# Kernel tuning notes

Hardware: AMD Instinct MI355X
Metric: run time of the kernel (lower is better)

The kernel has to match this reference:

```python
import jax, jax.numpy as jnp
import numpy as np

NE, NR = 200000, 500
D, TRI_H, TET_H = 128, 256, 256
NTRI, NTET = 500000, 200000
B = 8192
E_ET, E_TT, E_ETT = 1500000, 800000, 800000


def _mean_aggregate(src_idx, dst_idx, src, num_dst):
    # scatter-add of gathered messages, then divide by per-dst counts (0 -> 0)
    agg = jax.ops.segment_sum(src[src_idx], dst_idx, num_segments=num_dst)
    cnt = jax.ops.segment_sum(jnp.ones(src_idx.shape[0], dtype=src.dtype), dst_idx, num_segments=num_dst)
    return jnp.where((cnt > 0)[:, None], agg / jnp.maximum(cnt, 1.0)[:, None], 0.0)


def _layernorm(x, w, b, eps=1e-5):
    mu = jnp.mean(x, axis=-1, keepdims=True)
    var = jnp.mean((x - mu) ** 2, axis=-1, keepdims=True)
    return (x - mu) / jnp.sqrt(var + eps) * w + b


def setup_inputs():
    key = jax.random.key(0)
    ks = jax.random.split(key, 24)
    def xav(k, fan_out, fan_in):
        a = np.sqrt(6.0 / (fan_in + fan_out))
        return jax.random.uniform(k, (fan_out, fan_in), jnp.float32, -a, a)
    inp = {
        'entity_emb': xav(ks[0], NE, D),
        'relation_emb': xav(ks[1], NR, D),
        'g2_w1': xav(ks[2], TRI_H, D), 'g2_b1': jnp.zeros((TRI_H,), jnp.float32),
        'g2_w2': xav(ks[3], TRI_H, TRI_H), 'g2_b2': jnp.zeros((TRI_H,), jnp.float32),
        'g3_w1': xav(ks[4], TET_H, TRI_H), 'g3_b1': jnp.zeros((TET_H,), jnp.float32),
        'g3_w2': xav(ks[5], TET_H, TET_H), 'g3_b2': jnp.zeros((TET_H,), jnp.float32),
        'te_w': xav(ks[6], D, TET_H), 'te_b': jnp.zeros((D,), jnp.float32),
        'ln_w': jnp.ones((D,), jnp.float32), 'ln_b': jnp.zeros((D,), jnp.float32),
        'fusion_alpha': jnp.zeros((2,), jnp.float32),
        'gamma': jnp.array([12.0], jnp.float32),
        'triples': jax.random.randint(ks[7], (B, 3), 0, NR, jnp.int64 if jax.config.jax_enable_x64 else jnp.int32),
        'et_index': jax.random.randint(ks[8], (2, E_ET), 0, NE, jnp.int32),
        'tt_index': jax.random.randint(ks[9], (2, E_TT), 0, NTET, jnp.int32),
        'ent_tet_index': jax.random.randint(ks[10], (2, E_ETT), 0, NTET, jnp.int32),
        'num_triangles': NTRI,
        'num_tetras': NTET,
    }
    return inp


def reference(entity_emb, relation_emb, g2_w1, g2_b1, g2_w2, g2_b2,
              g3_w1, g3_b1, g3_w2, g3_b2, te_w, te_b, ln_w, ln_b,
              fusion_alpha, gamma, triples, et_index, tt_index,
              ent_tet_index, num_triangles, num_tetras):
    # gnn2: entity -> triangle  (segment-mean then Linear -> GELU -> Linear)
    tri_agg = _mean_aggregate(et_index[0], et_index[1], entity_emb, num_triangles)
    tri = jax.nn.gelu(tri_agg @ g2_w1.T + g2_b1, approximate=False) @ g2_w2.T + g2_b2
    # gnn3: triangle -> tetra
    tet_agg = _mean_aggregate(tt_index[0], tt_index[1], tri, num_tetras)
    tet = jax.nn.gelu(tet_agg @ g3_w1.T + g3_b1, approximate=False) @ g3_w2.T + g3_b2
    # project tetra -> entity dim, then tetra -> entity mean-aggregate (swapped index rows)
    tet_proj = tet @ te_w.T + te_b
    v_topo = _mean_aggregate(ent_tet_index[1], ent_tet_index[0], tet_proj, entity_emb.shape[0])
    v_topo = _layernorm(v_topo, ln_w, ln_b)
    # learned fusion
    w = jax.nn.softmax(fusion_alpha)
    V = w[0] * entity_emb + w[1] * v_topo
    # TransE scoring: gamma - ||V[h] + R[r] - V[t]||_2
    h, r, t = triples[:, 0], triples[:, 1], triples[:, 2]
    diff = V[h] + relation_emb[r] - V[t]
    return gamma[0] - jnp.sqrt(jnp.sum(diff * diff, axis=-1))
```

## Files before the change

### kernel.cpp

```cpp
#include <hip/hip_runtime.h>
#include <cmath>

#define NE_     200000
#define NR_     500
#define D_      128
#define TRIH_   256
#define TETH_   256
#define NTRI_   500000
#define NTET_   200000
#define B_      8192
#define EET_    1500000
#define ETT_    800000
#define EETT_   800000

#define CAP_V   2048
#define CAP_TP  8192
#define CAP_TRI 12288

#define LCAP_ET  131072
#define LCAP_TT  32768
#define LCAP_ETT 16384

#define COARSEN 8
#define CHUNK   (256 * COARSEN)

#define NBC_V   ((NE_   + CHUNK - 1) / CHUNK)
#define NBC_TP  ((NTET_ + CHUNK - 1) / CHUNK)
#define NBC_TRI ((NTRI_ + CHUNK - 1) / CHUNK)
#define NBF_ET  ((EET_  + CHUNK - 1) / CHUNK)
#define NBF_TT  ((ETT_  + CHUNK - 1) / CHUNK)
#define NBF_ETT ((EETT_ + CHUNK - 1) / CHUNK)
#define MARKB   1024


typedef float f32x4 __attribute__((ext_vector_type(4)));
typedef short s16x8 __attribute__((ext_vector_type(8)));

__device__ __forceinline__ float gelu_exact(float v) {
    return 0.5f * v * (1.0f + erff(v * 0.70710678118654752f));
}

__device__ __forceinline__ unsigned short f2bf(float f) {
    unsigned int u = __float_as_uint(f);
    unsigned int r = (u + 0x7fffu + ((u >> 16) & 1u)) >> 16;
    return (unsigned short)r;
}

__device__ __forceinline__ int wave_rank_emit(bool pred, int* lcnt, int lane) {
    unsigned long long mask = __ballot(pred);
    int rank = __popcll(mask & ((1ull << lane) - 1ull));
    int total = __popcll(mask);
    int wb = 0;
    if (lane == 0 && total) wb = atomicAdd(lcnt, total);
    wb = __shfl(wb, 0, 64);
    return pred ? (wb + rank) : -1;
}


__global__ void k_init_all(int* __restrict__ id_v, int* __restrict__ id_tp,
                           int* __restrict__ id_tri, int* __restrict__ ctr,
                           const float* __restrict__ w1, const float* __restrict__ w2,
                           const float* __restrict__ w3, const float* __restrict__ w4,
                           const float* __restrict__ w5, unsigned short* __restrict__ wb,
                           int* __restrict__ deg_tri, int* __restrict__ deg_tp,
                           int* __restrict__ deg_v) {
    int i = blockIdx.x * blockDim.x + threadIdx.x;
    int st = gridDim.x * blockDim.x;
    for (int x = i; x < NE_; x += st) id_v[x] = -1;
    for (int x = i; x < NTET_; x += st) id_tp[x] = -1;
    for (int x = i; x < NTRI_; x += st) id_tri[x] = -1;
    if (i < 16) ctr[i] = 0;
    for (int x = i; x < 262144; x += st) {
        float f;
        if (x < 32768)       f = w1[x];
        else if (x < 98304)  f = w2[x - 32768];
        else if (x < 163840) f = w3[x - 98304];
        else if (x < 229376) f = w4[x - 163840];
        else                 f = w5[x - 229376];
        wb[x] = f2bf(f);
    }
    for (int x = i; x < CAP_TRI; x += st) deg_tri[x] = 0;
    for (int x = i; x < CAP_TP; x += st) deg_tp[x] = 0;
    for (int x = i; x < CAP_V; x += st) deg_v[x] = 0;
}


__global__ void k_mark_v(const int* __restrict__ triples, int* __restrict__ id_v) {
    int b = blockIdx.x * blockDim.x + threadIdx.x;
    if (b >= B_) return;
    id_v[triples[b * 3 + 0]] = -2;
    id_v[triples[b * 3 + 2]] = -2;
}

__global__ void k_mark_tp(const int* __restrict__ ett, const int* __restrict__ id_v,
                          int* __restrict__ id_tp) {
    int i = blockIdx.x * blockDim.x + threadIdx.x;
    int st = gridDim.x * blockDim.x;
    for (int e = i; e < EETT_; e += st)
        if (id_v[ett[e]] != -1) id_tp[ett[EETT_ + e]] = -2;
}


__device__ void do_compact(int* __restrict__ arr, int n, int* __restrict__ g, int cap,
                           int bid, int* lcnt, int* lbase) {
    if (threadIdx.x == 0) *lcnt = 0;
    __syncthreads();
    const int lane = threadIdx.x & 63;
    const int base = bid * CHUNK;
    int pos[COARSEN];
#pragma unroll
    for (int u = 0; u < COARSEN; ++u) {
        int e = base + u * 256 + threadIdx.x;
        bool pred = (e < n) && (arr[e] == -2);
        pos[u] = wave_rank_emit(pred, lcnt, lane);
    }
    __syncthreads();
    if (threadIdx.x == 0) *lbase = *lcnt ? atomicAdd(g, *lcnt) : 0;
    __syncthreads();
    const int b0 = *lbase;
#pragma unroll
    for (int u = 0; u < COARSEN; ++u) {
        if (pos[u] >= 0) {
            int e = base + u * 256 + threadIdx.x;
            int idx = b0 + pos[u];
            arr[e] = (idx < cap) ? idx : -1;
        }
    }
}

__device__ void do_filter(const int* __restrict__ e0, const int* __restrict__ e1,
                          const int* __restrict__ map0, const int* __restrict__ map1,
                          int n, int2* __restrict__ list, int* __restrict__ nctr, int lcap,
                          int* __restrict__ deg, int bid, int* lcnt, int* lbase) {
    if (threadIdx.x == 0) *lcnt = 0;
    __syncthreads();
    const int lane = threadIdx.x & 63;
    const int base = bid * CHUNK;
    int pos[COARSEN]; int2 val[COARSEN];
#pragma unroll
    for (int u = 0; u < COARSEN; ++u) {
        int e = base + u * 256 + threadIdx.x;
        bool pred = false;
        int m1 = -1, src = -1;
        if (e < n) {
            m1 = map1[e1[e]];
            if (m1 >= 0) {
                src = map0 ? map0[e0[e]] : e0[e];
                pred = (src >= 0);
            }
        }
        pos[u] = wave_rank_emit(pred, lcnt, lane);
        if (pred) { val[u] = make_int2(src, m1); atomicAdd(&deg[m1], 1); }
    }
    __syncthreads();
    if (threadIdx.x == 0) *lbase = *lcnt ? atomicAdd(nctr, *lcnt) : 0;
    __syncthreads();
    const int b0 = *lbase;
#pragma unroll
    for (int u = 0; u < COARSEN; ++u)
        if (pos[u] >= 0 && b0 + pos[u] < lcap) list[b0 + pos[u]] = val[u];
}

__launch_bounds__(256)
__global__ void k_p4(const int* __restrict__ tt, int* __restrict__ id_v,
                     int* __restrict__ id_tp, int* __restrict__ id_tri,
                     int* __restrict__ ctr) {
    __shared__ int lcnt, lbase;
    int bid = blockIdx.x;
    if (bid < NBC_V) { do_compact(id_v, NE_, &ctr[0], CAP_V, bid, &lcnt, &lbase); return; }
    bid -= NBC_V;
    if (bid < NBC_TP) { do_compact(id_tp, NTET_, &ctr[1], CAP_TP, bid, &lcnt, &lbase); return; }
    bid -= NBC_TP;
    int i = bid * 256 + threadIdx.x;
    int st = MARKB * 256;
    for (int e = i; e < ETT_; e += st)
        if (id_tp[tt[ETT_ + e]] != -1) id_tri[tt[e]] = -2;
}

__launch_bounds__(256)
__global__ void k_p5(int* __restrict__ id_tri, const int* __restrict__ ett,
                     const int* __restrict__ id_v, const int* __restrict__ id_tp,
                     int2* __restrict__ list_ett, int* __restrict__ deg_v,
                     int* __restrict__ ctr) {
    __shared__ int lcnt, lbase;
    int bid = blockIdx.x;
    if (bid < NBC_TRI) { do_compact(id_tri, NTRI_, &ctr[2], CAP_TRI, bid, &lcnt, &lbase); return; }
    bid -= NBC_TRI;
    do_filter(ett + EETT_, ett, id_tp, id_v, EETT_, list_ett, &ctr[5], LCAP_ETT,
              deg_v, bid, &lcnt, &lbase);
}

__launch_bounds__(256)
__global__ void k_p6(const int* __restrict__ et, const int* __restrict__ tt,
                     const int* __restrict__ id_tri, const int* __restrict__ id_tp,
                     int2* __restrict__ list_et, int2* __restrict__ list_tt,
                     int* __restrict__ deg_tri, int* __restrict__ deg_tp,
                     int* __restrict__ ctr) {
    __shared__ int lcnt, lbase;
    int bid = blockIdx.x;
    if (bid < NBF_ET) {
        do_filter(et, et + EET_, nullptr, id_tri, EET_, list_et, &ctr[3], LCAP_ET,
                  deg_tri, bid, &lcnt, &lbase);
        return;
    }
    bid -= NBF_ET;
    do_filter(tt, tt + ETT_, id_tri, id_tp, ETT_, list_tt, &ctr[4], LCAP_TT,
              deg_tp, bid, &lcnt, &lbase);
}


__device__ void scan_level(const int* __restrict__ deg, int* __restrict__ start,
                           int* __restrict__ cur, int n) {
    __shared__ int wsum[16];
    const int tid = threadIdx.x;
    const int per = (n + 1023) >> 10;
    const int base = tid * per;
    int s = 0;
    for (int k = 0; k < per; ++k) { int i = base + k; if (i < n) s += deg[i]; }
    const int lane = tid & 63, wid = tid >> 6;
    int v = s;
#pragma unroll
    for (int o = 1; o < 64; o <<= 1) { int t = __shfl_up(v, o, 64); if (lane >= o) v += t; }
    if (lane == 63) wsum[wid] = v;
    __syncthreads();
    if (tid < 16) {
        int w = wsum[tid];
#pragma unroll
        for (int o = 1; o < 16; o <<= 1) { int t = __shfl_up(w, o, 64); if (tid >= o) w += t; }
        wsum[tid] = w;
    }
    __syncthreads();
    int run = v - s + (wid > 0 ? wsum[wid - 1] : 0);
    for (int k = 0; k < per; ++k) {
        int i = base + k;
        if (i < n) { start[i] = run; cur[i] = run; run += deg[i]; }
    }
    if (tid == 0) start[n] = wsum[15];
}

__global__ void k_scan(const int* __restrict__ deg_tri, int* __restrict__ st_tri, int* __restrict__ cu_tri,
                       const int* __restrict__ deg_tp, int* __restrict__ st_tp, int* __restrict__ cu_tp,
                       const int* __restrict__ deg_v, int* __restrict__ st_v, int* __restrict__ cu_v) {
    if (blockIdx.x == 0)      scan_level(deg_tri, st_tri, cu_tri, CAP_TRI);
    else if (blockIdx.x == 1) scan_level(deg_tp, st_tp, cu_tp, CAP_TP);
    else                      scan_level(deg_v, st_v, cu_v, CAP_V);
}

__global__ void k_bucket(const int* __restrict__ ctr,
                         const int2* __restrict__ le, int* __restrict__ cu_tri, int* __restrict__ be,
                         const int2* __restrict__ lt, int* __restrict__ cu_tp, int* __restrict__ btk,
                         const int2* __restrict__ lv, int* __restrict__ cu_v, int* __restrict__ bv) {
    int i = blockIdx.x * blockDim.x + threadIdx.x;
    int st = gridDim.x * blockDim.x;
    int n0 = min(ctr[3], LCAP_ET);
    for (int e = i; e < n0; e += st) {
        int2 p = le[e];
        int slot = atomicAdd(&cu_tri[p.y], 1);
        if (slot < LCAP_ET) be[slot] = p.x;
    }
    int n1 = min(ctr[4], LCAP_TT);
    for (int e = i; e < n1; e += st) {
        int2 p = lt[e];
        int slot = atomicAdd(&cu_tp[p.y], 1);
        if (slot < LCAP_TT) btk[slot] = p.x;
    }
    int n2 = min(ctr[5], LCAP_ETT);
    for (int e = i; e < n2; e += st) {
        int2 p = lv[e];
        int slot = atomicAdd(&cu_v[p.y], 1);
        if (slot < LCAP_ETT) bv[slot] = p.x;
    }
}


template<int W>
__global__ void k_gather(const int* __restrict__ ctrp, int cidx, int cap, int lcap,
                         const int* __restrict__ start, const int* __restrict__ bidx,
                         const float* __restrict__ src, unsigned srcN,
                         float* __restrict__ dst, float* __restrict__ cnt) {
    const int c = min(ctrp[cidx], cap);
    const int lane = threadIdx.x & 63;
    int row = (blockIdx.x * blockDim.x + threadIdx.x) >> 6;
    const int nw = (gridDim.x * blockDim.x) >> 6;
    for (; row < c; row += nw) {
        int s0 = min(start[row], lcap), s1 = min(start[row + 1], lcap);
        if (W == 128) {
            float2 acc = make_float2(0.f, 0.f);
            for (int e = s0; e < s1; ++e) {
                unsigned si = (unsigned)bidx[e];
                if (si < srcN) {
                    float2 v = ((const float2*)(src + (size_t)si * 128))[lane];
                    acc.x += v.x; acc.y += v.y;
                }
            }
            ((float2*)(dst + (size_t)row * 128))[lane] = acc;
        } else {
            float4 acc = make_float4(0.f, 0.f, 0.f, 0.f);
            for (int e = s0; e < s1; ++e) {
                unsigned si = (unsigned)bidx[e];
                if (si < srcN) {
                    float4 v = ((const float4*)(src + (size_t)si * 256))[lane];
                    acc.x += v.x; acc.y += v.y; acc.z += v.z; acc.w += v.w;
                }
            }
            ((float4*)(dst + (size_t)row * 256))[lane] = acc;
        }
        if (lane == 0) cnt[row] = (float)(s1 - s0);
    }
}


template<int K, int ACT, bool DIV>
__launch_bounds__(256)
__global__ void k_gemm(const int* __restrict__ ctrp, int ctr_idx, int cap,
                       const float* __restrict__ A, const float* __restrict__ cnt,
                       const unsigned short* __restrict__ Wb, const float* __restrict__ bias,
                       float* __restrict__ C, int N) {
    constexpr int KU = K / 8;
    __shared__ uint4 lA[32 * KU];
    __shared__ uint4 lW[32 * KU];
    __shared__ float invs[32];
    const int c = min(ctrp[ctr_idx], cap);
    const int row0 = blockIdx.x * 32;
    if (row0 >= c) return;
    const int tid = threadIdx.x;
    const int gc0 = blockIdx.y * 32;

    if (DIV) {
        if (tid < 32) {
            int gr = row0 + tid;
            float cc = (gr < c) ? cnt[gr] : 0.0f;
            invs[tid] = (cc > 0.0f) ? 1.0f / cc : 0.0f;
        }
        __syncthreads();
    }
#pragma unroll
    for (int it = 0; it < KU / 8; ++it) {
        int u = tid + it * 256;
        int r = u / KU, ku = u % KU;
        const float* src = &A[(size_t)(row0 + r) * K + ku * 8];
        float4 f0 = *(const float4*)src;
        float4 f1 = *(const float4*)(src + 4);
        float m = DIV ? invs[r] : 1.0f;
        s16x8 v;
        v[0] = (short)f2bf(f0.x * m); v[1] = (short)f2bf(f0.y * m);
        v[2] = (short)f2bf(f0.z * m); v[3] = (short)f2bf(f0.w * m);
        v[4] = (short)f2bf(f1.x * m); v[5] = (short)f2bf(f1.y * m);
        v[6] = (short)f2bf(f1.z * m); v[7] = (short)f2bf(f1.w * m);
        *(s16x8*)&lA[r * KU + (ku ^ (r & 7))] = v;
    }
#pragma unroll
    for (int it = 0; it < KU / 8; ++it) {
        int u = tid + it * 256;
        int r = u / KU, ku = u % KU;
        lW[r * KU + (ku ^ (r & 7))] = *(const uint4*)&Wb[(size_t)(gc0 + r) * K + ku * 8];
    }
    __syncthreads();

    const int w = tid >> 6, l = tid & 63;
    const int wr = (w >> 1) * 16, wc = (w & 1) * 16;
    const int fr = l & 15, fo = l >> 4;
    f32x4 acc = {0.0f, 0.0f, 0.0f, 0.0f};
    const uint4* pa = &lA[(wr + fr) * KU];
    const uint4* pb = &lW[(wc + fr) * KU];
    const int sa = fr & 7, sb = fr & 7;
#pragma unroll
    for (int kk = 0; kk < K / 32; ++kk) {
        s16x8 a = *(const s16x8*)&pa[(kk * 4 + fo) ^ sa];
        s16x8 b = *(const s16x8*)&pb[(kk * 4 + fo) ^ sb];
        acc = __builtin_amdgcn_mfma_f32_16x16x32_bf16(a, b, acc, 0, 0, 0);
    }
    const int gcol = gc0 + wc + fr;
    const float bb = bias[gcol];
#pragma unroll
    for (int j = 0; j < 4; ++j) {
        int grow = row0 + wr + fo * 4 + j;
        if (grow < c) {
            float v = acc[j] + bb;
            if (ACT == 1) v = gelu_exact(v);
            C[(size_t)grow * N + gcol] = v;
        }
    }
}


__global__ void k_final(const float* __restrict__ emb, const float* __restrict__ rel,
                        const float* __restrict__ v_topo, const float* __restrict__ cnt_v,
                        const int* __restrict__ id_v, const float* __restrict__ ln_w,
                        const float* __restrict__ ln_b, const float* __restrict__ alpha,
                        const float* __restrict__ gamma, const int* __restrict__ triples,
                        float* __restrict__ out) {
    const int lane = threadIdx.x & 63;
    const int b = blockIdx.x * 4 + (threadIdx.x >> 6);
    if (b >= B_) return;
    float a0 = alpha[0], a1 = alpha[1];
    float m = fmaxf(a0, a1);
    float e0 = expf(a0 - m), e1 = expf(a1 - m);
    float w0 = e0 / (e0 + e1), w1 = e1 / (e0 + e1);
    int h = triples[b * 3 + 0];
    int r = triples[b * 3 + 1];
    int t = triples[b * 3 + 2];
    int jh = max(id_v[h], 0);
    int jt = max(id_v[t], 0);
    const float2* vt2 = (const float2*)v_topo;
    float2 rh = vt2[(size_t)jh * 64 + lane];
    float2 rt = vt2[(size_t)jt * 64 + lane];
    float chn = cnt_v[jh], ctn = cnt_v[jt];
    float ih = (chn > 0.f) ? 1.f / chn : 0.f;
    float it_ = (ctn > 0.f) ? 1.f / ctn : 0.f;
    float2 xh = make_float2(rh.x * ih, rh.y * ih);
    float2 xt = make_float2(rt.x * it_, rt.y * it_);
    float sh = xh.x + xh.y, st = xt.x + xt.y;
#pragma unroll
    for (int o = 32; o >= 1; o >>= 1) { sh += __shfl_xor(sh, o, 64); st += __shfl_xor(st, o, 64); }
    float muh = sh * (1.f / 128.f), mut = st * (1.f / 128.f);
    float2 dh = make_float2(xh.x - muh, xh.y - muh);
    float2 dt = make_float2(xt.x - mut, xt.y - mut);
    float vh_ = dh.x * dh.x + dh.y * dh.y, vt_ = dt.x * dt.x + dt.y * dt.y;
#pragma unroll
    for (int o = 32; o >= 1; o >>= 1) { vh_ += __shfl_xor(vh_, o, 64); vt_ += __shfl_xor(vt_, o, 64); }
    float rsh = rsqrtf(vh_ * (1.f / 128.f) + 1e-5f);
    float rst = rsqrtf(vt_ * (1.f / 128.f) + 1e-5f);
    float2 lw = ((const float2*)ln_w)[lane];
    float2 lb = ((const float2*)ln_b)[lane];
    float2 lnh = make_float2(dh.x * rsh * lw.x + lb.x, dh.y * rsh * lw.y + lb.y);
    float2 lnt = make_float2(dt.x * rst * lw.x + lb.x, dt.y * rst * lw.y + lb.y);
    float2 eh = ((const float2*)emb)[(size_t)h * 64 + lane];
    float2 etv = ((const float2*)emb)[(size_t)t * 64 + lane];
    float2 rr = ((const float2*)rel)[(size_t)r * 64 + lane];
    float dx = (w0 * eh.x + w1 * lnh.x) + rr.x - (w0 * etv.x + w1 * lnt.x);
    float dy = (w0 * eh.y + w1 * lnh.y) + rr.y - (w0 * etv.y + w1 * lnt.y);
    float ss = dx * dx + dy * dy;
#pragma unroll
    for (int o = 32; o >= 1; o >>= 1) ss += __shfl_xor(ss, o, 64);
    if (lane == 0) out[b] = gamma[0] - sqrtf(ss);
}


extern "C" void kernel_launch(void* const* d_in, const int* in_sizes, int n_in,
                              void* d_out, int out_size, void* d_ws, size_t ws_size,
                              hipStream_t stream) {
    const float* entity_emb = (const float*)d_in[0];
    const float* relation_emb = (const float*)d_in[1];
    const float* g2_w1 = (const float*)d_in[2];
    const float* g2_b1 = (const float*)d_in[3];
    const float* g2_w2 = (const float*)d_in[4];
    const float* g2_b2 = (const float*)d_in[5];
    const float* g3_w1 = (const float*)d_in[6];
    const float* g3_b1 = (const float*)d_in[7];
    const float* g3_w2 = (const float*)d_in[8];
    const float* g3_b2 = (const float*)d_in[9];
    const float* te_w = (const float*)d_in[10];
    const float* te_b = (const float*)d_in[11];
    const float* ln_w = (const float*)d_in[12];
    const float* ln_b = (const float*)d_in[13];
    const float* alpha = (const float*)d_in[14];
    const float* gamma = (const float*)d_in[15];
    const int* triples = (const int*)d_in[16];
    const int* et = (const int*)d_in[17];
    const int* tt = (const int*)d_in[18];
    const int* ett = (const int*)d_in[19];
    float* out = (float*)d_out;

    char* base = (char*)d_ws;
    size_t off = 0;
    auto take = [&](size_t bytes) -> void* {
        void* p = base + off;
        off = (off + bytes + 255) & ~(size_t)255;
        return p;
    };
    int* id_v = (int*)take((size_t)NE_ * 4);
    int* id_tp = (int*)take((size_t)NTET_ * 4);
    int* id_tri = (int*)take((size_t)NTRI_ * 4);
    int* ctr = (int*)take(64);
    int* deg_tri = (int*)take((size_t)CAP_TRI * 4);
    int* deg_tp = (int*)take((size_t)CAP_TP * 4);
    int* deg_v = (int*)take((size_t)CAP_V * 4);
    int* st_tri = (int*)take((size_t)(CAP_TRI + 1) * 4);
    int* st_tp = (int*)take((size_t)(CAP_TP + 1) * 4);
    int* st_v = (int*)take((size_t)(CAP_V + 1) * 4);
    int* cu_tri = (int*)take((size_t)CAP_TRI * 4);
    int* cu_tp = (int*)take((size_t)CAP_TP * 4);
    int* cu_v = (int*)take((size_t)CAP_V * 4);
    float* cnt_tri = (float*)take((size_t)CAP_TRI * 4);
    float* cnt_tp = (float*)take((size_t)CAP_TP * 4);
    float* cnt_v = (float*)take((size_t)CAP_V * 4);
    float* tri_agg = (float*)take((size_t)CAP_TRI * D_ * 4);
    float* h_tri = (float*)take((size_t)CAP_TRI * TRIH_ * 4);
    float* tri_c = (float*)take((size_t)CAP_TRI * TRIH_ * 4);
    float* tet_agg = (float*)take((size_t)CAP_TP * TRIH_ * 4);
    float* h_tet = (float*)take((size_t)CAP_TP * TETH_ * 4);
    float* tet_proj = (float*)take((size_t)CAP_TP * D_ * 4);
    float* v_topo = (float*)take((size_t)CAP_V * D_ * 4);
    unsigned short* wb = (unsigned short*)take((size_t)262144 * 2);
    int2* list_et = (int2*)take((size_t)LCAP_ET * 8);
    int2* list_tt = (int2*)take((size_t)LCAP_TT * 8);
    int2* list_ett = (int2*)take((size_t)LCAP_ETT * 8);
    int* b_et = (int*)take((size_t)LCAP_ET * 4);
    int* b_tt = (int*)take((size_t)LCAP_TT * 4);
    int* b_ett = (int*)take((size_t)LCAP_ETT * 4);
    if (off > ws_size) return;

    float* y_tet = h_tri;
    const unsigned short* wb_g2w1 = wb;
    const unsigned short* wb_g2w2 = wb + 32768;
    const unsigned short* wb_g3w1 = wb + 98304;
    const unsigned short* wb_g3w2 = wb + 163840;
    const unsigned short* wb_te   = wb + 229376;

    k_init_all<<<2048, 256, 0, stream>>>(id_v, id_tp, id_tri, ctr,
                                         g2_w1, g2_w2, g3_w1, g3_w2, te_w, wb,
                                         deg_tri, deg_tp, deg_v);
    k_mark_v<<<(B_ + 255) / 256, 256, 0, stream>>>(triples, id_v);
    k_mark_tp<<<MARKB, 256, 0, stream>>>(ett, id_v, id_tp);
    k_p4<<<NBC_V + NBC_TP + MARKB, 256, 0, stream>>>(tt, id_v, id_tp, id_tri, ctr);
    k_p5<<<NBC_TRI + NBF_ETT, 256, 0, stream>>>(id_tri, ett, id_v, id_tp, list_ett, deg_v, ctr);
    k_p6<<<NBF_ET + NBF_TT, 256, 0, stream>>>(et, tt, id_tri, id_tp, list_et, list_tt,
                                              deg_tri, deg_tp, ctr);
    k_scan<<<3, 1024, 0, stream>>>(deg_tri, st_tri, cu_tri, deg_tp, st_tp, cu_tp,
                                   deg_v, st_v, cu_v);
    k_bucket<<<256, 256, 0, stream>>>(ctr, list_et, cu_tri, b_et,
                                      list_tt, cu_tp, b_tt, list_ett, cu_v, b_ett);

    k_gather<128><<<2048, 256, 0, stream>>>(ctr, 2, CAP_TRI, LCAP_ET, st_tri, b_et,
                                            entity_emb, NE_, tri_agg, cnt_tri);
    dim3 gtri(CAP_TRI / 32, TRIH_ / 32);
    k_gemm<128, 1, true><<<gtri, 256, 0, stream>>>(ctr, 2, CAP_TRI, tri_agg, cnt_tri,
                                                   wb_g2w1, g2_b1, h_tri, TRIH_);
    k_gemm<256, 0, false><<<gtri, 256, 0, stream>>>(ctr, 2, CAP_TRI, h_tri, nullptr,
                                                    wb_g2w2, g2_b2, tri_c, TRIH_);
    k_gather<256><<<512, 256, 0, stream>>>(ctr, 1, CAP_TP, LCAP_TT, st_tp, b_tt,
                                           tri_c, CAP_TRI, tet_agg, cnt_tp);
    dim3 gtet(CAP_TP / 32, TETH_ / 32);
    k_gemm<256, 1, true><<<gtet, 256, 0, stream>>>(ctr, 1, CAP_TP, tet_agg, cnt_tp,
                                                   wb_g3w1, g3_b1, h_tet, TETH_);
    k_gemm<256, 0, false><<<gtet, 256, 0, stream>>>(ctr, 1, CAP_TP, h_tet, nullptr,
                                                    wb_g3w2, g3_b2, y_tet, TETH_);
    dim3 gproj(CAP_TP / 32, D_ / 32);
    k_gemm<256, 0, false><<<gproj, 256, 0, stream>>>(ctr, 1, CAP_TP, y_tet, nullptr,
                                                     wb_te, te_b, tet_proj, D_);
    k_gather<128><<<128, 256, 0, stream>>>(ctr, 0, CAP_V, LCAP_ETT, st_v, b_ett,
                                           tet_proj, CAP_TP, v_topo, cnt_v);
    k_final<<<(B_ + 3) / 4, 256, 0, stream>>>(entity_emb, relation_emb, v_topo, cnt_v, id_v,
                                              ln_w, ln_b, alpha, gamma, triples, out);
}
```

Measured before the change: 135.8 us.

## Assign compact ids via CAS and fuse MLP stages into fewer kernels

The mark-then-compact passes over full entity, tetra and triangle arrays are replaced by atomicCAS-based on-the-fly id assignment, which removes the chunked compaction kernels. The three edge filters are merged into one launch. The triangle MLP (two GEMMs with GELU) is fused into one kernel that keeps the hidden tile in LDS. The tetra gather plus its two GEMMs and the projection are fused into one kernel, and the final entity gather moves into the scoring kernel. Fused kernels recompute the first-layer hidden tile for every output column block, and the CAS assignment makes id order nondeterministic and adds atomic contention.

```diff
diff --git a/kernel.cpp b/kernel.cpp
--- a/kernel.cpp
+++ b/kernel.cpp
@@ -23,14 +23,16 @@
 
 #define COARSEN 8
 #define CHUNK   (256 * COARSEN)
-
-#define NBC_V   ((NE_   + CHUNK - 1) / CHUNK)
-#define NBC_TP  ((NTET_ + CHUNK - 1) / CHUNK)
-#define NBC_TRI ((NTRI_ + CHUNK - 1) / CHUNK)
 #define NBF_ET  ((EET_  + CHUNK - 1) / CHUNK)
 #define NBF_TT  ((ETT_  + CHUNK - 1) / CHUNK)
 #define NBF_ETT ((EETT_ + CHUNK - 1) / CHUNK)
 #define MARKB   1024
+
+#define WB_G2W1 0
+#define WB_G2W2 32768
+#define WB_G3W1 98304
+#define WB_G3W2 163840
+#define WB_TE   229376
 
 
 typedef float f32x4 __attribute__((ext_vector_type(4)));
@@ -56,14 +58,22 @@
     return pred ? (wb + rank) : -1;
 }
 
-
-__global__ void k_init_all(int* __restrict__ id_v, int* __restrict__ id_tp,
-                           int* __restrict__ id_tri, int* __restrict__ ctr,
-                           const float* __restrict__ w1, const float* __restrict__ w2,
-                           const float* __restrict__ w3, const float* __restrict__ w4,
-                           const float* __restrict__ w5, unsigned short* __restrict__ wb,
-                           int* __restrict__ deg_tri, int* __restrict__ deg_tp,
-                           int* __restrict__ deg_v) {
+__device__ __forceinline__ void cas_assign(int* arr, int x, int* g, int cap) {
+    int old = atomicCAS(&arr[x], -1, -3);
+    if (old == -1) {
+        int id = atomicAdd(g, 1);
+        arr[x] = (id < cap) ? id : -1;
+    }
+}
+
+
+__global__ void k_init(int* __restrict__ id_v, int* __restrict__ id_tp,
+                       int* __restrict__ id_tri, int* __restrict__ ctr,
+                       const float* __restrict__ w1, const float* __restrict__ w2,
+                       const float* __restrict__ w3, const float* __restrict__ w4,
+                       const float* __restrict__ w5, unsigned short* __restrict__ wb,
+                       int* __restrict__ deg_tri, int* __restrict__ deg_tp,
+                       int* __restrict__ deg_v) {
     int i = blockIdx.x * blockDim.x + threadIdx.x;
     int st = gridDim.x * blockDim.x;
     for (int x = i; x < NE_; x += st) id_v[x] = -1;
@@ -85,48 +95,30 @@
 }
 
 
-__global__ void k_mark_v(const int* __restrict__ triples, int* __restrict__ id_v) {
+__global__ void k_cas_v(const int* __restrict__ triples, int* __restrict__ id_v,
+                        int* __restrict__ ctr) {
     int b = blockIdx.x * blockDim.x + threadIdx.x;
     if (b >= B_) return;
-    id_v[triples[b * 3 + 0]] = -2;
-    id_v[triples[b * 3 + 2]] = -2;
-}
-
-__global__ void k_mark_tp(const int* __restrict__ ett, const int* __restrict__ id_v,
-                          int* __restrict__ id_tp) {
+    cas_assign(id_v, triples[b * 3 + 0], &ctr[0], CAP_V);
+    cas_assign(id_v, triples[b * 3 + 2], &ctr[0], CAP_V);
+}
+
+__global__ void k_cas_tp(const int* __restrict__ ett, const int* __restrict__ id_v,
+                         int* __restrict__ id_tp, int* __restrict__ ctr) {
     int i = blockIdx.x * blockDim.x + threadIdx.x;
     int st = gridDim.x * blockDim.x;
     for (int e = i; e < EETT_; e += st)
-        if (id_v[ett[e]] != -1) id_tp[ett[EETT_ + e]] = -2;
-}
-
-
-__device__ void do_compact(int* __restrict__ arr, int n, int* __restrict__ g, int cap,
-                           int bid, int* lcnt, int* lbase) {
-    if (threadIdx.x == 0) *lcnt = 0;
-    __syncthreads();
-    const int lane = threadIdx.x & 63;
-    const int base = bid * CHUNK;
-    int pos[COARSEN];
-#pragma unroll
-    for (int u = 0; u < COARSEN; ++u) {
-        int e = base + u * 256 + threadIdx.x;
-        bool pred = (e < n) && (arr[e] == -2);
-        pos[u] = wave_rank_emit(pred, lcnt, lane);
-    }
-    __syncthreads();
-    if (threadIdx.x == 0) *lbase = *lcnt ? atomicAdd(g, *lcnt) : 0;
-    __syncthreads();
-    const int b0 = *lbase;
-#pragma unroll
-    for (int u = 0; u < COARSEN; ++u) {
-        if (pos[u] >= 0) {
-            int e = base + u * 256 + threadIdx.x;
-            int idx = b0 + pos[u];
-            arr[e] = (idx < cap) ? idx : -1;
-        }
-    }
-}
+        if (id_v[ett[e]] >= 0) cas_assign(id_tp, ett[EETT_ + e], &ctr[1], CAP_TP);
+}
+
+__global__ void k_cas_tri(const int* __restrict__ tt, const int* __restrict__ id_tp,
+                          int* __restrict__ id_tri, int* __restrict__ ctr) {
+    int i = blockIdx.x * blockDim.x + threadIdx.x;
+    int st = gridDim.x * blockDim.x;
+    for (int e = i; e < ETT_; e += st)
+        if (id_tp[tt[ETT_ + e]] >= 0) cas_assign(id_tri, tt[e], &ctr[2], CAP_TRI);
+}
+
 
 __device__ void do_filter(const int* __restrict__ e0, const int* __restrict__ e1,
                           const int* __restrict__ map0, const int* __restrict__ map1,
@@ -162,40 +154,14 @@
 }
 
 __launch_bounds__(256)
-__global__ void k_p4(const int* __restrict__ tt, int* __restrict__ id_v,
-                     int* __restrict__ id_tp, int* __restrict__ id_tri,
-                     int* __restrict__ ctr) {
-    __shared__ int lcnt, lbase;
-    int bid = blockIdx.x;
-    if (bid < NBC_V) { do_compact(id_v, NE_, &ctr[0], CAP_V, bid, &lcnt, &lbase); return; }
-    bid -= NBC_V;
-    if (bid < NBC_TP) { do_compact(id_tp, NTET_, &ctr[1], CAP_TP, bid, &lcnt, &lbase); return; }
-    bid -= NBC_TP;
-    int i = bid * 256 + threadIdx.x;
-    int st = MARKB * 256;
-    for (int e = i; e < ETT_; e += st)
-        if (id_tp[tt[ETT_ + e]] != -1) id_tri[tt[e]] = -2;
-}
-
-__launch_bounds__(256)
-__global__ void k_p5(int* __restrict__ id_tri, const int* __restrict__ ett,
-                     const int* __restrict__ id_v, const int* __restrict__ id_tp,
-                     int2* __restrict__ list_ett, int* __restrict__ deg_v,
-                     int* __restrict__ ctr) {
-    __shared__ int lcnt, lbase;
-    int bid = blockIdx.x;
-    if (bid < NBC_TRI) { do_compact(id_tri, NTRI_, &ctr[2], CAP_TRI, bid, &lcnt, &lbase); return; }
-    bid -= NBC_TRI;
-    do_filter(ett + EETT_, ett, id_tp, id_v, EETT_, list_ett, &ctr[5], LCAP_ETT,
-              deg_v, bid, &lcnt, &lbase);
-}
-
-__launch_bounds__(256)
-__global__ void k_p6(const int* __restrict__ et, const int* __restrict__ tt,
-                     const int* __restrict__ id_tri, const int* __restrict__ id_tp,
-                     int2* __restrict__ list_et, int2* __restrict__ list_tt,
-                     int* __restrict__ deg_tri, int* __restrict__ deg_tp,
-                     int* __restrict__ ctr) {
+__global__ void k_filter3(const int* __restrict__ et, const int* __restrict__ tt,
+                          const int* __restrict__ ett,
+                          const int* __restrict__ id_tri, const int* __restrict__ id_tp,
+                          const int* __restrict__ id_v,
+                          int2* __restrict__ list_et, int2* __restrict__ list_tt,
+                          int2* __restrict__ list_ett,
+                          int* __restrict__ deg_tri, int* __restrict__ deg_tp,
+                          int* __restrict__ deg_v, int* __restrict__ ctr) {
     __shared__ int lcnt, lbase;
     int bid = blockIdx.x;
     if (bid < NBF_ET) {
@@ -204,8 +170,14 @@
         return;
     }
     bid -= NBF_ET;
-    do_filter(tt, tt + ETT_, id_tri, id_tp, ETT_, list_tt, &ctr[4], LCAP_TT,
-              deg_tp, bid, &lcnt, &lbase);
+    if (bid < NBF_TT) {
+        do_filter(tt, tt + ETT_, id_tri, id_tp, ETT_, list_tt, &ctr[4], LCAP_TT,
+                  deg_tp, bid, &lcnt, &lbase);
+        return;
+    }
+    bid -= NBF_TT;
+    do_filter(ett + EETT_, ett, id_tp, id_v, EETT_, list_ett, &ctr[5], LCAP_ETT,
+              deg_v, bid, &lcnt, &lbase);
 }
 
 
@@ -273,123 +245,218 @@
 }
 
 
-template<int W>
-__global__ void k_gather(const int* __restrict__ ctrp, int cidx, int cap, int lcap,
-                         const int* __restrict__ start, const int* __restrict__ bidx,
-                         const float* __restrict__ src, unsigned srcN,
-                         float* __restrict__ dst, float* __restrict__ cnt) {
-    const int c = min(ctrp[cidx], cap);
+__global__ void k_gather_tri(const int* __restrict__ ctr, const int* __restrict__ st,
+                             const int* __restrict__ bidx, const float* __restrict__ emb,
+                             float* __restrict__ tri_agg) {
+    const int c = min(ctr[2], CAP_TRI);
     const int lane = threadIdx.x & 63;
     int row = (blockIdx.x * blockDim.x + threadIdx.x) >> 6;
     const int nw = (gridDim.x * blockDim.x) >> 6;
     for (; row < c; row += nw) {
-        int s0 = min(start[row], lcap), s1 = min(start[row + 1], lcap);
-        if (W == 128) {
-            float2 acc = make_float2(0.f, 0.f);
-            for (int e = s0; e < s1; ++e) {
-                unsigned si = (unsigned)bidx[e];
-                if (si < srcN) {
-                    float2 v = ((const float2*)(src + (size_t)si * 128))[lane];
-                    acc.x += v.x; acc.y += v.y;
-                }
+        int s0 = min(st[row], LCAP_ET), s1 = min(st[row + 1], LCAP_ET);
+        float2 acc = make_float2(0.f, 0.f);
+        for (int e = s0; e < s1; ++e) {
+            unsigned si = (unsigned)bidx[e];
+            if (si < NE_) {
+                float2 v = ((const float2*)(emb + (size_t)si * 128))[lane];
+                acc.x += v.x; acc.y += v.y;
             }
-            ((float2*)(dst + (size_t)row * 128))[lane] = acc;
-        } else {
-            float4 acc = make_float4(0.f, 0.f, 0.f, 0.f);
-            for (int e = s0; e < s1; ++e) {
-                unsigned si = (unsigned)bidx[e];
-                if (si < srcN) {
-                    float4 v = ((const float4*)(src + (size_t)si * 256))[lane];
-                    acc.x += v.x; acc.y += v.y; acc.z += v.z; acc.w += v.w;
-                }
-            }
-            ((float4*)(dst + (size_t)row * 256))[lane] = acc;
-        }
-        if (lane == 0) cnt[row] = (float)(s1 - s0);
-    }
-}
-
-
-template<int K, int ACT, bool DIV>
+        }
+        float inv = (s1 > s0) ? 1.f / (float)(s1 - s0) : 0.f;
+        acc.x *= inv; acc.y *= inv;
+        ((float2*)(tri_agg + (size_t)row * 128))[lane] = acc;
+    }
+}
+
+
+template<int KU>
+__device__ __forceinline__ f32x4 tile_mma(const unsigned short* xs, const unsigned short* ws,
+                                          int ra, int rb, int fo) {
+    f32x4 acc = {0.f, 0.f, 0.f, 0.f};
+    const uint4* pa = (const uint4*)xs + ra * KU;
+    const uint4* pb = (const uint4*)ws + rb * KU;
+    const int sa = ra & 7, sb = rb & 7;
+#pragma unroll
+    for (int kk = 0; kk < KU / 4; ++kk) {
+        s16x8 a = *(const s16x8*)&pa[(kk * 4 + fo) ^ sa];
+        s16x8 b = *(const s16x8*)&pb[(kk * 4 + fo) ^ sb];
+        acc = __builtin_amdgcn_mfma_f32_16x16x32_bf16(a, b, acc, 0, 0, 0);
+    }
+    return acc;
+}
+
+
 __launch_bounds__(256)
-__global__ void k_gemm(const int* __restrict__ ctrp, int ctr_idx, int cap,
-                       const float* __restrict__ A, const float* __restrict__ cnt,
-                       const unsigned short* __restrict__ Wb, const float* __restrict__ bias,
-                       float* __restrict__ C, int N) {
-    constexpr int KU = K / 8;
-    __shared__ uint4 lA[32 * KU];
-    __shared__ uint4 lW[32 * KU];
-    __shared__ float invs[32];
-    const int c = min(ctrp[ctr_idx], cap);
+__global__ void k_tri_mlp(const int* __restrict__ ctr, const float* __restrict__ agg,
+                          const unsigned short* __restrict__ wb,
+                          const float* __restrict__ b1, const float* __restrict__ b2,
+                          float* __restrict__ tri_c) {
+    __shared__ __align__(16) unsigned short xs[32 * 16 * 8];
+    __shared__ __align__(16) unsigned short hs[32 * 32 * 8];
+    __shared__ __align__(16) unsigned short ws[32 * 32 * 8];
+    const int c = min(ctr[2], CAP_TRI);
     const int row0 = blockIdx.x * 32;
     if (row0 >= c) return;
     const int tid = threadIdx.x;
-    const int gc0 = blockIdx.y * 32;
-
-    if (DIV) {
-        if (tid < 32) {
-            int gr = row0 + tid;
-            float cc = (gr < c) ? cnt[gr] : 0.0f;
-            invs[tid] = (cc > 0.0f) ? 1.0f / cc : 0.0f;
-        }
-        __syncthreads();
-    }
-#pragma unroll
-    for (int it = 0; it < KU / 8; ++it) {
-        int u = tid + it * 256;
-        int r = u / KU, ku = u % KU;
-        const float* src = &A[(size_t)(row0 + r) * K + ku * 8];
-        float4 f0 = *(const float4*)src;
-        float4 f1 = *(const float4*)(src + 4);
-        float m = DIV ? invs[r] : 1.0f;
+#pragma unroll
+    for (int it = 0; it < 2; ++it) {
+        int u = tid + it * 256, r = u >> 4, ku = u & 15;
+        int gr = row0 + r;
         s16x8 v;
-        v[0] = (short)f2bf(f0.x * m); v[1] = (short)f2bf(f0.y * m);
-        v[2] = (short)f2bf(f0.z * m); v[3] = (short)f2bf(f0.w * m);
-        v[4] = (short)f2bf(f1.x * m); v[5] = (short)f2bf(f1.y * m);
-        v[6] = (short)f2bf(f1.z * m); v[7] = (short)f2bf(f1.w * m);
-        *(s16x8*)&lA[r * KU + (ku ^ (r & 7))] = v;
-    }
-#pragma unroll
-    for (int it = 0; it < KU / 8; ++it) {
-        int u = tid + it * 256;
-        int r = u / KU, ku = u % KU;
-        lW[r * KU + (ku ^ (r & 7))] = *(const uint4*)&Wb[(size_t)(gc0 + r) * K + ku * 8];
-    }
-    __syncthreads();
-
+        if (gr < c) {
+            const float* src = &agg[(size_t)gr * 128 + ku * 8];
+#pragma unroll
+            for (int q = 0; q < 8; ++q) v[q] = (short)f2bf(src[q]);
+        } else {
+#pragma unroll
+            for (int q = 0; q < 8; ++q) v[q] = 0;
+        }
+        *(s16x8*)&xs[((r << 4) + (ku ^ (r & 7))) * 8] = v;
+    }
+    __syncthreads();
     const int w = tid >> 6, l = tid & 63;
     const int wr = (w >> 1) * 16, wc = (w & 1) * 16;
     const int fr = l & 15, fo = l >> 4;
-    f32x4 acc = {0.0f, 0.0f, 0.0f, 0.0f};
-    const uint4* pa = &lA[(wr + fr) * KU];
-    const uint4* pb = &lW[(wc + fr) * KU];
-    const int sa = fr & 7, sb = fr & 7;
-#pragma unroll
-    for (int kk = 0; kk < K / 32; ++kk) {
-        s16x8 a = *(const s16x8*)&pa[(kk * 4 + fo) ^ sa];
-        s16x8 b = *(const s16x8*)&pb[(kk * 4 + fo) ^ sb];
-        acc = __builtin_amdgcn_mfma_f32_16x16x32_bf16(a, b, acc, 0, 0, 0);
-    }
-    const int gcol = gc0 + wc + fr;
-    const float bb = bias[gcol];
+    for (int cc8 = 0; cc8 < 8; ++cc8) {
+#pragma unroll
+        for (int it = 0; it < 2; ++it) {
+            int u = tid + it * 256, r = u >> 4, ku = u & 15;
+            *(uint4*)&ws[((r << 4) + (ku ^ (r & 7))) * 8] =
+                *(const uint4*)&wb[WB_G2W1 + (size_t)(cc8 * 32 + r) * 128 + ku * 8];
+        }
+        __syncthreads();
+        f32x4 acc = tile_mma<16>(xs, ws, wr + fr, wc + fr, fo);
+        int col = cc8 * 32 + wc + fr;
+        float bb = b1[col];
+        int unit = col >> 3, off = col & 7;
+#pragma unroll
+        for (int j = 0; j < 4; ++j) {
+            int row = wr + fo * 4 + j;
+            hs[((row << 5) + (unit ^ (row & 7))) * 8 + off] = f2bf(gelu_exact(acc[j] + bb));
+        }
+        __syncthreads();
+    }
+    const int oc = blockIdx.y;
+#pragma unroll
+    for (int it = 0; it < 4; ++it) {
+        int u = tid + it * 256, r = u >> 5, ku = u & 31;
+        *(uint4*)&ws[((r << 5) + (ku ^ (r & 7))) * 8] =
+            *(const uint4*)&wb[WB_G2W2 + (size_t)(oc * 32 + r) * 256 + ku * 8];
+    }
+    __syncthreads();
+    f32x4 acc = tile_mma<32>(hs, ws, wr + fr, wc + fr, fo);
+    int col = oc * 32 + wc + fr;
+    float bb = b2[col];
 #pragma unroll
     for (int j = 0; j < 4; ++j) {
         int grow = row0 + wr + fo * 4 + j;
-        if (grow < c) {
-            float v = acc[j] + bb;
-            if (ACT == 1) v = gelu_exact(v);
-            C[(size_t)grow * N + gcol] = v;
-        }
+        if (grow < c) tri_c[(size_t)grow * 256 + col] = acc[j] + bb;
+    }
+}
+
+
+__launch_bounds__(256)
+__global__ void k_tet_mlp(const int* __restrict__ ctr, const int* __restrict__ st,
+                          const int* __restrict__ bidx, const float* __restrict__ tri_c,
+                          const unsigned short* __restrict__ wb,
+                          const float* __restrict__ b1, const float* __restrict__ b2,
+                          const float* __restrict__ bt, float* __restrict__ tet_proj) {
+    __shared__ __align__(16) unsigned short xs[32 * 32 * 8];
+    __shared__ __align__(16) unsigned short hs[32 * 32 * 8];
+    __shared__ __align__(16) unsigned short ws[32 * 32 * 8];
+    const int c = min(ctr[1], CAP_TP);
+    const int row0 = blockIdx.x * 32;
+    if (row0 >= c) return;
+    const int tid = threadIdx.x, lane = tid & 63, wv = tid >> 6;
+    for (int rr = wv * 8; rr < wv * 8 + 8; ++rr) {
+        int row = row0 + rr;
+        float a0 = 0.f, a1 = 0.f, a2 = 0.f, a3 = 0.f;
+        int d = 0;
+        if (row < c) {
+            int s0 = min(st[row], LCAP_TT), s1 = min(st[row + 1], LCAP_TT);
+            d = s1 - s0;
+            for (int e = s0; e < s1; ++e) {
+                unsigned si = (unsigned)bidx[e];
+                if (si < CAP_TRI) {
+                    float4 v = ((const float4*)(tri_c + (size_t)si * 256))[lane];
+                    a0 += v.x; a1 += v.y; a2 += v.z; a3 += v.w;
+                }
+            }
+        }
+        float inv = (d > 0) ? 1.f / (float)d : 0.f;
+        unsigned lo = (unsigned)f2bf(a0 * inv) | ((unsigned)f2bf(a1 * inv) << 16);
+        unsigned hi = (unsigned)f2bf(a2 * inv) | ((unsigned)f2bf(a3 * inv) << 16);
+        int col0 = lane * 4;
+        int ku = col0 >> 3, off = col0 & 7;
+        *(uint2*)&xs[((rr << 5) + (ku ^ (rr & 7))) * 8 + off] = make_uint2(lo, hi);
+    }
+    __syncthreads();
+    const int w = tid >> 6;
+    const int wr = (w >> 1) * 16, wc = (w & 1) * 16;
+    const int fr = lane & 15, fo = lane >> 4;
+    for (int cc8 = 0; cc8 < 8; ++cc8) {
+#pragma unroll
+        for (int it = 0; it < 4; ++it) {
+            int u = tid + it * 256, r = u >> 5, ku = u & 31;
+            *(uint4*)&ws[((r << 5) + (ku ^ (r & 7))) * 8] =
+                *(const uint4*)&wb[WB_G3W1 + (size_t)(cc8 * 32 + r) * 256 + ku * 8];
+        }
+        __syncthreads();
+        f32x4 acc = tile_mma<32>(xs, ws, wr + fr, wc + fr, fo);
+        int col = cc8 * 32 + wc + fr;
+        float bb = b1[col];
+        int unit = col >> 3, off = col & 7;
+#pragma unroll
+        for (int j = 0; j < 4; ++j) {
+            int row = wr + fo * 4 + j;
+            hs[((row << 5) + (unit ^ (row & 7))) * 8 + off] = f2bf(gelu_exact(acc[j] + bb));
+        }
+        __syncthreads();
+    }
+    for (int cc8 = 0; cc8 < 8; ++cc8) {
+#pragma unroll
+        for (int it = 0; it < 4; ++it) {
+            int u = tid + it * 256, r = u >> 5, ku = u & 31;
+            *(uint4*)&ws[((r << 5) + (ku ^ (r & 7))) * 8] =
+                *(const uint4*)&wb[WB_G3W2 + (size_t)(cc8 * 32 + r) * 256 + ku * 8];
+        }
+        __syncthreads();
+        f32x4 acc = tile_mma<32>(hs, ws, wr + fr, wc + fr, fo);
+        int col = cc8 * 32 + wc + fr;
+        float bb = b2[col];
+        int unit = col >> 3, off = col & 7;
+#pragma unroll
+        for (int j = 0; j < 4; ++j) {
+            int row = wr + fo * 4 + j;
+            xs[((row << 5) + (unit ^ (row & 7))) * 8 + off] = f2bf(acc[j] + bb);
+        }
+        __syncthreads();
+    }
+    const int oc = blockIdx.y;
+#pragma unroll
+    for (int it = 0; it < 4; ++it) {
+        int u = tid + it * 256, r = u >> 5, ku = u & 31;
+        *(uint4*)&ws[((r << 5) + (ku ^ (r & 7))) * 8] =
+            *(const uint4*)&wb[WB_TE + (size_t)(oc * 32 + r) * 256 + ku * 8];
+    }
+    __syncthreads();
+    f32x4 acc = tile_mma<32>(xs, ws, wr + fr, wc + fr, fo);
+    int col = oc * 32 + wc + fr;
+    float bb = bt[col];
+#pragma unroll
+    for (int j = 0; j < 4; ++j) {
+        int grow = row0 + wr + fo * 4 + j;
+        if (grow < c) tet_proj[(size_t)grow * 128 + col] = acc[j] + bb;
     }
 }
 
 
 __global__ void k_final(const float* __restrict__ emb, const float* __restrict__ rel,
-                        const float* __restrict__ v_topo, const float* __restrict__ cnt_v,
-                        const int* __restrict__ id_v, const float* __restrict__ ln_w,
-                        const float* __restrict__ ln_b, const float* __restrict__ alpha,
-                        const float* __restrict__ gamma, const int* __restrict__ triples,
-                        float* __restrict__ out) {
+                        const float* __restrict__ tet_proj, const int* __restrict__ st_v,
+                        const int* __restrict__ b_ett, const int* __restrict__ id_v,
+                        const float* __restrict__ lnw, const float* __restrict__ lnb,
+                        const float* __restrict__ alpha, const float* __restrict__ gamma,
+                        const int* __restrict__ triples, float* __restrict__ out) {
     const int lane = threadIdx.x & 63;
     const int b = blockIdx.x * 4 + (threadIdx.x >> 6);
     if (b >= B_) return;
@@ -400,16 +467,34 @@
     int h = triples[b * 3 + 0];
     int r = triples[b * 3 + 1];
     int t = triples[b * 3 + 2];
-    int jh = max(id_v[h], 0);
-    int jt = max(id_v[t], 0);
-    const float2* vt2 = (const float2*)v_topo;
-    float2 rh = vt2[(size_t)jh * 64 + lane];
-    float2 rt = vt2[(size_t)jt * 64 + lane];
-    float chn = cnt_v[jh], ctn = cnt_v[jt];
-    float ih = (chn > 0.f) ? 1.f / chn : 0.f;
-    float it_ = (ctn > 0.f) ? 1.f / ctn : 0.f;
-    float2 xh = make_float2(rh.x * ih, rh.y * ih);
-    float2 xt = make_float2(rt.x * it_, rt.y * it_);
+    int jh = id_v[h]; jh = (jh >= 0 && jh < CAP_V) ? jh : 0;
+    int jt = id_v[t]; jt = (jt >= 0 && jt < CAP_V) ? jt : 0;
+
+    float2 xh = make_float2(0.f, 0.f), xt = make_float2(0.f, 0.f);
+    {
+        int s0 = min(st_v[jh], LCAP_ETT), s1 = min(st_v[jh + 1], LCAP_ETT);
+        for (int e = s0; e < s1; ++e) {
+            unsigned si = (unsigned)b_ett[e];
+            if (si < CAP_TP) {
+                float2 v = ((const float2*)(tet_proj + (size_t)si * 128))[lane];
+                xh.x += v.x; xh.y += v.y;
+            }
+        }
+        float inv = (s1 > s0) ? 1.f / (float)(s1 - s0) : 0.f;
+        xh.x *= inv; xh.y *= inv;
+    }
+    {
+        int s0 = min(st_v[jt], LCAP_ETT), s1 = min(st_v[jt + 1], LCAP_ETT);
+        for (int e = s0; e < s1; ++e) {
+            unsigned si = (unsigned)b_ett[e];
+            if (si < CAP_TP) {
+                float2 v = ((const float2*)(tet_proj + (size_t)si * 128))[lane];
+                xt.x += v.x; xt.y += v.y;
+            }
+        }
+        float inv = (s1 > s0) ? 1.f / (float)(s1 - s0) : 0.f;
+        xt.x *= inv; xt.y *= inv;
+    }
     float sh = xh.x + xh.y, st = xt.x + xt.y;
 #pragma unroll
     for (int o = 32; o >= 1; o >>= 1) { sh += __shfl_xor(sh, o, 64); st += __shfl_xor(st, o, 64); }
@@ -421,8 +506,8 @@
     for (int o = 32; o >= 1; o >>= 1) { vh_ += __shfl_xor(vh_, o, 64); vt_ += __shfl_xor(vt_, o, 64); }
     float rsh = rsqrtf(vh_ * (1.f / 128.f) + 1e-5f);
     float rst = rsqrtf(vt_ * (1.f / 128.f) + 1e-5f);
-    float2 lw = ((const float2*)ln_w)[lane];
-    float2 lb = ((const float2*)ln_b)[lane];
+    float2 lw = ((const float2*)lnw)[lane];
+    float2 lb = ((const float2*)lnb)[lane];
     float2 lnh = make_float2(dh.x * rsh * lw.x + lb.x, dh.y * rsh * lw.y + lb.y);
     float2 lnt = make_float2(dt.x * rst * lw.x + lb.x, dt.y * rst * lw.y + lb.y);
     float2 eh = ((const float2*)emb)[(size_t)h * 64 + lane];
@@ -482,16 +567,6 @@
     int* cu_tri = (int*)take((size_t)CAP_TRI * 4);
     int* cu_tp = (int*)take((size_t)CAP_TP * 4);
     int* cu_v = (int*)take((size_t)CAP_V * 4);
-    float* cnt_tri = (float*)take((size_t)CAP_TRI * 4);
-    float* cnt_tp = (float*)take((size_t)CAP_TP * 4);
-    float* cnt_v = (float*)take((size_t)CAP_V * 4);
-    float* tri_agg = (float*)take((size_t)CAP_TRI * D_ * 4);
-    float* h_tri = (float*)take((size_t)CAP_TRI * TRIH_ * 4);
-    float* tri_c = (float*)take((size_t)CAP_TRI * TRIH_ * 4);
-    float* tet_agg = (float*)take((size_t)CAP_TP * TRIH_ * 4);
-    float* h_tet = (float*)take((size_t)CAP_TP * TETH_ * 4);
-    float* tet_proj = (float*)take((size_t)CAP_TP * D_ * 4);
-    float* v_topo = (float*)take((size_t)CAP_V * D_ * 4);
     unsigned short* wb = (unsigned short*)take((size_t)262144 * 2);
     int2* list_et = (int2*)take((size_t)LCAP_ET * 8);
     int2* list_tt = (int2*)take((size_t)LCAP_TT * 8);
@@ -499,48 +574,31 @@
     int* b_et = (int*)take((size_t)LCAP_ET * 4);
     int* b_tt = (int*)take((size_t)LCAP_TT * 4);
     int* b_ett = (int*)take((size_t)LCAP_ETT * 4);
+    float* tri_agg = (float*)take((size_t)CAP_TRI * D_ * 4);
+    float* tri_c = (float*)take((size_t)CAP_TRI * TRIH_ * 4);
+    float* tet_proj = (float*)take((size_t)CAP_TP * D_ * 4);
     if (off > ws_size) return;
 
-    float* y_tet = h_tri;
-    const unsigned short* wb_g2w1 = wb;
-    const unsigned short* wb_g2w2 = wb + 32768;
-    const unsigned short* wb_g3w1 = wb + 98304;
-    const unsigned short* wb_g3w2 = wb + 163840;
-    const unsigned short* wb_te   = wb + 229376;
-
-    k_init_all<<<2048, 256, 0, stream>>>(id_v, id_tp, id_tri, ctr,
-                                         g2_w1, g2_w2, g3_w1, g3_w2, te_w, wb,
-                                         deg_tri, deg_tp, deg_v);
-    k_mark_v<<<(B_ + 255) / 256, 256, 0, stream>>>(triples, id_v);
-    k_mark_tp<<<MARKB, 256, 0, stream>>>(ett, id_v, id_tp);
-    k_p4<<<NBC_V + NBC_TP + MARKB, 256, 0, stream>>>(tt, id_v, id_tp, id_tri, ctr);
-    k_p5<<<NBC_TRI + NBF_ETT, 256, 0, stream>>>(id_tri, ett, id_v, id_tp, list_ett, deg_v, ctr);
-    k_p6<<<NBF_ET + NBF_TT, 256, 0, stream>>>(et, tt, id_tri, id_tp, list_et, list_tt,
-                                              deg_tri, deg_tp, ctr);
+    k_init<<<2048, 256, 0, stream>>>(id_v, id_tp, id_tri, ctr,
+                                     g2_w1, g2_w2, g3_w1, g3_w2, te_w, wb,
+                                     deg_tri, deg_tp, deg_v);
+    k_cas_v<<<(B_ + 255) / 256, 256, 0, stream>>>(triples, id_v, ctr);
+    k_cas_tp<<<MARKB, 256, 0, stream>>>(ett, id_v, id_tp, ctr);
+    k_cas_tri<<<MARKB, 256, 0, stream>>>(tt, id_tp, id_tri, ctr);
+    k_filter3<<<NBF_ET + NBF_TT + NBF_ETT, 256, 0, stream>>>(
+        et, tt, ett, id_tri, id_tp, id_v,
+        list_et, list_tt, list_ett, deg_tri, deg_tp, deg_v, ctr);
     k_scan<<<3, 1024, 0, stream>>>(deg_tri, st_tri, cu_tri, deg_tp, st_tp, cu_tp,
                                    deg_v, st_v, cu_v);
     k_bucket<<<256, 256, 0, stream>>>(ctr, list_et, cu_tri, b_et,
                                       list_tt, cu_tp, b_tt, list_ett, cu_v, b_ett);
-
-    k_gather<128><<<2048, 256, 0, stream>>>(ctr, 2, CAP_TRI, LCAP_ET, st_tri, b_et,
-                                            entity_emb, NE_, tri_agg, cnt_tri);
-    dim3 gtri(CAP_TRI / 32, TRIH_ / 32);
-    k_gemm<128, 1, true><<<gtri, 256, 0, stream>>>(ctr, 2, CAP_TRI, tri_agg, cnt_tri,
-                                                   wb_g2w1, g2_b1, h_tri, TRIH_);
-    k_gemm<256, 0, false><<<gtri, 256, 0, stream>>>(ctr, 2, CAP_TRI, h_tri, nullptr,
-                                                    wb_g2w2, g2_b2, tri_c, TRIH_);
-    k_gather<256><<<512, 256, 0, stream>>>(ctr, 1, CAP_TP, LCAP_TT, st_tp, b_tt,
-                                           tri_c, CAP_TRI, tet_agg, cnt_tp);
-    dim3 gtet(CAP_TP / 32, TETH_ / 32);
-    k_gemm<256, 1, true><<<gtet, 256, 0, stream>>>(ctr, 1, CAP_TP, tet_agg, cnt_tp,
-                                                   wb_g3w1, g3_b1, h_tet, TETH_);
-    k_gemm<256, 0, false><<<gtet, 256, 0, stream>>>(ctr, 1, CAP_TP, h_tet, nullptr,
-                                                    wb_g3w2, g3_b2, y_tet, TETH_);
-    dim3 gproj(CAP_TP / 32, D_ / 32);
-    k_gemm<256, 0, false><<<gproj, 256, 0, stream>>>(ctr, 1, CAP_TP, y_tet, nullptr,
-                                                     wb_te, te_b, tet_proj, D_);
-    k_gather<128><<<128, 256, 0, stream>>>(ctr, 0, CAP_V, LCAP_ETT, st_v, b_ett,
-                                           tet_proj, CAP_TP, v_topo, cnt_v);
-    k_final<<<(B_ + 3) / 4, 256, 0, stream>>>(entity_emb, relation_emb, v_topo, cnt_v, id_v,
-                                              ln_w, ln_b, alpha, gamma, triples, out);
-}
+    k_gather_tri<<<2048, 256, 0, stream>>>(ctr, st_tri, b_et, entity_emb, tri_agg);
+    dim3 gtri(CAP_TRI / 32, 8);
+    k_tri_mlp<<<gtri, 256, 0, stream>>>(ctr, tri_agg, wb, g2_b1, g2_b2, tri_c);
+    dim3 gtet(CAP_TP / 32, 4);
+    k_tet_mlp<<<gtet, 256, 0, stream>>>(ctr, st_tp, b_tt, tri_c, wb,
+                                        g3_b1, g3_b2, te_b, tet_proj);
+    k_final<<<(B_ + 3) / 4, 256, 0, stream>>>(entity_emb, relation_emb, tet_proj,
+                                              st_v, b_ett, id_v, ln_w, ln_b,
+                                              alpha, gamma, triples, out);
+}
```

New measurement: 250.6 us. 84.6% more time.
